# Kernel tuning notes

Hardware: AMD Instinct MI355X
Metric: run time of the kernel (lower is better)

The kernel has to match this reference:

```python
import jax, jax.numpy as jnp
import numpy as np

B, L, K = 16, 512, 30          # proteins, residues per protein, kNN neighbors
N = B * L
H, FC = 32, 3                  # h_channels, frame_channels
C = H + FC                     # fused sphere channels (35)
HEADS, AC, VC = 8, 16, 8       # heads, alpha channels (H//2), value channels (H//4)
RBF_N, POS_N = 16, 16
EF = RBF_N + POS_N

# idealized backbone atom positions (N, CA, C) in the local residue frame
IDEAL_BB = np.array([[-0.525, 1.363, 0.0], [0.0, 0.0, 0.0], [1.526, 0.0, 0.0]], dtype=np.float32)
# cartesian (x,y,z) -> real-SH l=1 ordering (y,z,x)
P_SH = np.array([[0., 1., 0.], [0., 0., 1.], [1., 0., 0.]], dtype=np.float32)


def _knn_edges(trans):
    # per-chain brute-force kNN (chains are contiguous blocks of length L)
    X = trans.reshape(B, L, 3)
    d2 = jnp.sum((X[:, :, None, :] - X[:, None, :, :]) ** 2, axis=-1)  # [B,L,L]
    d2 = d2 + jnp.eye(L, dtype=d2.dtype) * 1e9                          # exclude self
    _, idx = jax.lax.top_k(-d2, K)                                      # [B,L,K]
    off = (jnp.arange(B) * L)[:, None, None]
    src = (idx + off).reshape(-1)              # neighbor (edge_index[0])
    tgt = jnp.repeat(jnp.arange(N), K)         # center   (edge_index[1])
    return src, tgt


def _edge_rot_mat(vec):
    # rotation aligning the edge vector with the y axis (eSCN init_edge_rot_mat style)
    nx = vec / (jnp.linalg.norm(vec, axis=-1, keepdims=True) + 1e-12)
    ref = jnp.where(jnp.abs(nx[:, :1]) < 0.9,
                    jnp.array([1., 0., 0.], dtype=vec.dtype),
                    jnp.array([0., 0., 1.], dtype=vec.dtype))
    nz = jnp.cross(nx, ref)
    nz = nz / (jnp.linalg.norm(nz, axis=-1, keepdims=True) + 1e-12)
    ny = jnp.cross(nx, nz)
    ny = ny / (jnp.linalg.norm(ny, axis=-1, keepdims=True) + 1e-12)
    return jnp.stack([nz, nx, ny], axis=-2)  # [E,3,3]


def _rbf(d, d_min=0.0, d_max=20.0, count=RBF_N):
    mu = jnp.linspace(d_min, d_max, count)
    sigma = (d_max - d_min) / count
    return jnp.exp(-(((d[:, None] - mu) / sigma) ** 2))


def _pos_emb(src, tgt, num=POS_N):
    d = (src - tgt).astype(jnp.float32)
    freq = jnp.exp(jnp.arange(0, num, 2, dtype=jnp.float32) * (-np.log(10000.0) / num))
    ang = d[:, None] * freq
    return jnp.concatenate([jnp.cos(ang), jnp.sin(ang)], axis=-1)


def _forward(rots, trans, node_emb, batch, x_mask, noising_mask,
             W_alpha, a_vec, W_v, W_o, W_g, W_2):
    src, tgt = _knn_edges(trans)
    vec = trans[src] - trans[tgt]
    dist = jnp.linalg.norm(vec, axis=-1)
    valid = jnp.isfinite(dist) & (dist > 1e-3)  # edge_select, applied as mask

    R = _edge_rot_mat(vec)
    P = jnp.asarray(P_SH)
    D1 = jnp.einsum('ij,ejk,lk->eil', P, R, P)  # l=1 Wigner in real-SH basis [E,3,3]

    edge_features = jnp.concatenate([_rbf(dist), _pos_emb(src, tgt)], axis=-1)  # [E,32]

    # fuse node features with backbone frame atoms and editability flag
    frame_atoms = jnp.einsum('nij,aj->nai', rots, jnp.asarray(IDEAL_BB))  # [N,3atoms,3xyz]
    editable = noising_mask & (~x_mask)
    emb = jnp.zeros((N, 4, C), dtype=node_emb.dtype)
    emb = emb.at[:, :, :H].set(node_emb)
    emb = emb.at[:, 1:4, H:].set(jnp.swapaxes(frame_atoms, -1, -2))
    emb = emb.at[:, 0, C - 1].set(editable.astype(node_emb.dtype))

    # gather + rotate source features into edge frames
    xs = emb[src]                                                   # [E,4,C]
    xs_rot = jnp.concatenate([xs[:, :1], jnp.einsum('eij,ejc->eic', D1, xs[:, 1:])], axis=1)

    # invariant attention logits (l=0 of rotated src, l=0 of tgt, edge feats)
    inv = jnp.concatenate([xs_rot[:, 0], emb[tgt, 0], edge_features], axis=-1)  # [E,102]
    hdn = jax.nn.silu(inv @ W_alpha).reshape(-1, HEADS, AC)
    logits = jax.nn.leaky_relu(jnp.einsum('ehk,hk->eh', hdn, a_vec), 0.2)
    logits = jnp.where(valid[:, None], logits, -1e9)

    # segment softmax over incoming edges of each target node
    mx = jax.lax.stop_gradient(jax.ops.segment_max(logits, tgt, num_segments=N))
    ex = jnp.exp(logits - mx[tgt]) * valid[:, None].astype(logits.dtype)
    den = jax.ops.segment_sum(ex, tgt, num_segments=N)
    alpha = ex / (den[tgt] + 1e-9)                                  # [E,HEADS]

    # equivariant values, attention-weighted, rotate back, scatter
    v = (xs_rot @ W_v).reshape(-1, 4, HEADS, VC)
    m = (v * alpha[:, None, :, None]).reshape(-1, 4, HEADS * VC)
    m = jnp.concatenate([m[:, :1], jnp.einsum('eji,ejc->eic', D1, m[:, 1:])], axis=1)  # D^T
    agg = jax.ops.segment_sum(m, tgt, num_segments=N)               # [N,4,64]

    y = agg @ W_o                                                    # [N,4,H]
    gate = jax.nn.silu(y[:, 0] @ W_g)                                # invariant gating FFN
    return (y * gate[:, None, :]) @ W_2                              # [N,4,H]


def setup_inputs():
    key = jax.random.key(0)
    ks = jax.random.split(key, 12)
    rots = jax.vmap(lambda m: jnp.linalg.qr(m)[0])(jax.random.normal(ks[0], (N, 3, 3)))
    trans = jax.random.normal(ks[1], (N, 3)) * 10.0
    node_emb = jax.random.normal(ks[2], (N, 4, H))
    batch = jnp.repeat(jnp.arange(B, dtype=jnp.int32), L)
    x_mask = jax.random.randint(ks[3], (N,), 0, 2).astype(bool)
    noising_mask = jax.random.randint(ks[4], (N,), 0, 2).astype(bool)
    s = lambda k, sh, fan: jax.random.normal(k, sh) / np.sqrt(fan)
    return dict(rots=rots, trans=trans, node_emb=node_emb, batch=batch,
                x_mask=x_mask, noising_mask=noising_mask,
                W_alpha=s(ks[5], (2 * C + EF, HEADS * AC), 2 * C + EF),
                a_vec=s(ks[6], (HEADS, AC), AC),
                W_v=s(ks[7], (C, HEADS * VC), C),
                W_o=s(ks[8], (HEADS * VC, H), HEADS * VC),
                W_g=s(ks[9], (H, H), H),
                W_2=s(ks[10], (H, H), H))


def reference(rots, trans, node_emb, batch, x_mask, noising_mask,
              W_alpha, a_vec, W_v, W_o, W_g, W_2):
    return _forward(rots, trans, node_emb, batch, x_mask, noising_mask,
                    W_alpha, a_vec, W_v, W_o, W_g, W_2)
```

## Files before the change

kernel.cpp:

```cpp
#include <hip/hip_runtime.h>
#include <cstdint>

#define B_ 16
#define L_ 512
#define N_ 8192
#define K_ 30
#define E_ (N_*K_)
#define H_ 32
#define C_ 35

typedef uint16_t u16;
typedef uint32_t u32;
typedef unsigned long long u64;
typedef float f2v __attribute__((ext_vector_type(2)));

static __device__ __forceinline__ f2v splat2(float x) { f2v v; v.x = x; v.y = x; return v; }

static __device__ __forceinline__ float ldf(const void* p, int i, int bf) {
    return bf ? __uint_as_float(((u32)((const u16*)p)[i]) << 16)
              : ((const float*)p)[i];
}
static __device__ __forceinline__ float bfu16(u16 x) {
    return __uint_as_float(((u32)x) << 16);
}
static __device__ __forceinline__ int ldmask(const void* p, int i, int mode) {
    if (mode == 0) return ((const unsigned char*)p)[i] != 0;
    if (mode == 2) return ((const u32*)p)[2*i] != 0;
    return ((const u32*)p)[i] != 0;
}
static __device__ __forceinline__ u16 f2bf(float f) {
    u32 x = __float_as_uint(f);
    u32 r = x + 0x7FFFu + ((x >> 16) & 1u);
    return (u16)(r >> 16);
}
static __device__ __forceinline__ float fsilu(float x) {
    return x * __builtin_amdgcn_rcpf(1.f + __expf(-x));
}
static __device__ __forceinline__ float RL(float x, int i) {
    return __uint_as_float((u32)__builtin_amdgcn_readlane((int)__float_as_uint(x), i));
}

static __device__ __forceinline__ int detect_bf(const void* tr, int lane) {
    const u16* p = (const u16*)tr;
    int cnt = 0;
    for (int i = lane; i < 256; i += 64) {
        u16 v = p[2 * i];
        int e = (v >> 7) & 0xFF;
        if ((e >= 100 && e <= 141) || (v & 0x7FFFu) == 0) cnt++;
    }
    #pragma unroll
    for (int d = 1; d < 64; d <<= 1) cnt += __shfl_xor(cnt, d, 64);
    return cnt >= 192;
}
static __device__ __forceinline__ int detect_mm(const void* xmv, int lane) {
    const u32* xm = (const u32*)xmv;
    int anyBig = 0, oddNZ = 0;
    for (int i = lane; i < 1024; i += 64) {
        u32 w = xm[i];
        if (w & ~1u) anyBig = 1;
        if ((i & 1) && w) oddNZ = 1;
    }
    #pragma unroll
    for (int d = 1; d < 64; d <<= 1) {
        anyBig |= __shfl_xor(anyBig, d, 64);
        oddNZ  |= __shfl_xor(oddNZ, d, 64);
    }
    return anyBig ? 0 : (oddNZ ? 1 : 2);
}

__constant__ float cBB[9] = {-0.525f, 1.363f, 0.f,  0.f, 0.f, 0.f,  1.526f, 0.f, 0.f};

#define DPP_UMIN(var, CTRL) \
    { u32 o_ = (u32)__builtin_amdgcn_update_dpp((int)(var), (int)(var), CTRL, 0xF, 0xF, false); \
      (var) = (o_ < (var)) ? o_ : (var); }
#define DPP_UMIN_ALL(var) \
    DPP_UMIN(var, 0x111) DPP_UMIN(var, 0x112) DPP_UMIN(var, 0x114) \
    DPP_UMIN(var, 0x118) DPP_UMIN(var, 0x142) DPP_UMIN(var, 0x143)

#define DPP_ADD8(part) \
    part += __uint_as_float((u32)__builtin_amdgcn_update_dpp( \
        (int)__float_as_uint(part), (int)__float_as_uint(part), 0xB1, 0xF, 0xF, false)); \
    part += __uint_as_float((u32)__builtin_amdgcn_update_dpp( \
        (int)__float_as_uint(part), (int)__float_as_uint(part), 0x4E, 0xF, 0xF, false)); \
    part += __uint_as_float((u32)__builtin_amdgcn_update_dpp( \
        (int)__float_as_uint(part), (int)__float_as_uint(part), 0x141, 0xF, 0xF, false));

#define PKFMA_LO(acc, rr, w) \
    asm("v_pk_fma_f32 %0, %1, %2, %0 op_sel:[0,0,0] op_sel_hi:[0,1,1]" \
        : "+v"(acc) : "v"(rr), "v"(w))
#define PKFMA_HI(acc, rr, w) \
    asm("v_pk_fma_f32 %0, %1, %2, %0 op_sel:[1,0,0] op_sel_hi:[1,1,1]" \
        : "+v"(acc) : "v"(rr), "v"(w))

__global__ __launch_bounds__(256) void knn_prep_kernel(
    const void* __restrict__ rots, const void* __restrict__ trans,
    const void* __restrict__ node,
    const void* __restrict__ xm, const void* __restrict__ nm,
    const void* __restrict__ Wa, const void* __restrict__ av,
    const void* __restrict__ Wv, const void* __restrict__ Wo,
    const void* __restrict__ Wg, const void* __restrict__ W2,
    int* __restrict__ flag, int* __restrict__ srcArr,
    float* __restrict__ hsrc, float* __restrict__ htgt,
    float* __restrict__ ptab, float* __restrict__ V,
    float* __restrict__ c_wrb, float* __restrict__ c_av,
    float* __restrict__ c_Wo, float* __restrict__ c_Wg, float* __restrict__ c_W2)
{
    __shared__ float sX[L_], sY[L_], sZ[L_];
    __shared__ int flagS[2];
    const int bid = blockIdx.x, tid = threadIdx.x;
    const int lane = tid & 63, wid = tid >> 6;

    if (wid == 0) {
        int bfv = detect_bf(trans, lane);
        int mmv = 0;
        if (bid == 0 || (bid >= 2048 && bid < 4096)) mmv = detect_mm(xm, lane);
        if (bid == 0 && lane == 0) { flag[0] = bfv; flag[1] = mmv; }
        if (lane == 0) { flagS[0] = bfv; flagS[1] = mmv; }
    }
    __syncthreads();
    const int bf = flagS[0];

    if (bid < 2048) {
        const int t0 = bid * 4;
        const int base = (t0 >> 9) << 9;
        if (bf) {
            const u16* tp = (const u16*)trans;
            for (int i = tid; i < L_; i += 256) {
                sX[i] = bfu16(tp[(base + i) * 3 + 0]);
                sY[i] = bfu16(tp[(base + i) * 3 + 1]);
                sZ[i] = bfu16(tp[(base + i) * 3 + 2]);
            }
        } else {
            const float* tp = (const float*)trans;
            for (int i = tid; i < L_; i += 256) {
                sX[i] = tp[(base + i) * 3 + 0];
                sY[i] = tp[(base + i) * 3 + 1];
                sZ[i] = tp[(base + i) * 3 + 2];
            }
        }
        __syncthreads();

        const int t = t0 + wid;
        const int l = t & 511;
        const float tx = sX[l], ty = sY[l], tz = sZ[l];

        u32 d2b[8];
        #pragma unroll
        for (int i = 0; i < 8; ++i) {
            int j = lane + (i << 6);
            float dx = __fsub_rn(tx, sX[j]);
            float dy = __fsub_rn(ty, sY[j]);
            float dz = __fsub_rn(tz, sZ[j]);
            float d2 = __fadd_rn(__fadd_rn(__fmul_rn(dx, dx), __fmul_rn(dy, dy)), __fmul_rn(dz, dz));
            if (j == l) d2 = __fadd_rn(d2, 1e9f);
            d2b[i] = __float_as_uint(d2);
        }

        int myres = 0;
        for (int k = 0; k < K_; ++k) {
            u32 bb = d2b[0]; int bs = 0;
            #pragma unroll
            for (int i = 1; i < 8; ++i)
                if (d2b[i] < bb) { bb = d2b[i]; bs = i; }
            u32 m = bb;
            DPP_UMIN_ALL(m)
            u32 gbits = (u32)__builtin_amdgcn_readlane((int)m, 63);
            u64 mask = __ballot(bb == gbits);
            u32 gidx;
            if (__popcll(mask) == 1) {
                int wl = __ffsll((long long)mask) - 1;
                gidx = (u32)__builtin_amdgcn_readlane((int)((bs << 6) | lane), wl);
            } else {
                u32 cand = (bb == gbits) ? (u32)((bs << 6) | lane) : 0xFFFFFFFFu;
                DPP_UMIN_ALL(cand)
                gidx = (u32)__builtin_amdgcn_readlane((int)cand, 63);
            }
            if (lane == (u32)k) myres = (int)(gidx & 511u);
            if ((gidx & 63u) == (u32)lane) {
                int ws = (int)(gidx >> 6);
                #pragma unroll
                for (int i = 0; i < 8; ++i)
                    if (ws == i) d2b[i] = 0xFFFFFFFFu;
            }
        }
        if (lane < K_) srcArr[t * K_ + lane] = base + myres;

    } else if (bid < 4096) {
        const int mm = flagS[1];
        const int n = (bid - 2048) * 4 + wid;

        float eA, eB, eC = 0.f;
        {
            int s = lane;
            int r = s / 35, c = s - r * 35;
            if (c < H_)      eA = ldf(node, n * 128 + r * 32 + c, bf);
            else if (r == 0) eA = (c == 34) ? ((ldmask(nm, n, mm) && !ldmask(xm, n, mm)) ? 1.f : 0.f) : 0.f;
            else {
                int i = r - 1, a = c - 32;
                eA = ldf(rots, n*9 + i*3 + 0, bf) * cBB[a*3 + 0]
                   + ldf(rots, n*9 + i*3 + 1, bf) * cBB[a*3 + 1]
                   + ldf(rots, n*9 + i*3 + 2, bf) * cBB[a*3 + 2];
            }
            s = lane + 64;
            r = s / 35; c = s - r * 35;
            if (c < H_)      eB = ldf(node, n * 128 + r * 32 + c, bf);
            else {
                int i = r - 1, a = c - 32;
                eB = ldf(rots, n*9 + i*3 + 0, bf) * cBB[a*3 + 0]
                   + ldf(rots, n*9 + i*3 + 1, bf) * cBB[a*3 + 1]
                   + ldf(rots, n*9 + i*3 + 2, bf) * cBB[a*3 + 2];
            }
            if (lane < 12) {
                s = lane + 128;
                r = s / 35; c = s - r * 35;
                if (c < H_)      eC = ldf(node, n * 128 + r * 32 + c, bf);
                else {
                    int i = r - 1, a = c - 32;
                    eC = ldf(rots, n*9 + i*3 + 0, bf) * cBB[a*3 + 0]
                       + ldf(rots, n*9 + i*3 + 1, bf) * cBB[a*3 + 1]
                       + ldf(rots, n*9 + i*3 + 2, bf) * cBB[a*3 + 2];
                }
            }
        }

        float a0 = 0.f, a1 = 0.f, b0 = 0.f, b1 = 0.f;
        float v0 = 0.f, v1 = 0.f, v2 = 0.f, v3 = 0.f;
        if (bf) {
            const u16* wa = (const u16*)Wa;
            const u16* wv = (const u16*)Wv;
            #pragma unroll
            for (int i = 0; i < 35; ++i) {
                float ei = RL(eA, i);
                a0 = fmaf(ei, bfu16(wa[i * 128 + lane]),        a0);
                a1 = fmaf(ei, bfu16(wa[i * 128 + lane + 64]),   a1);
                b0 = fmaf(ei, bfu16(wa[(35 + i) * 128 + lane]),      b0);
                b1 = fmaf(ei, bfu16(wa[(35 + i) * 128 + lane + 64]), b1);
            }
            #pragma unroll
            for (int cp = 0; cp < 35; ++cp) {
                float w = bfu16(wv[cp * 64 + lane]);
                float e1 = (35 + cp < 64) ? RL(eA, 35 + cp) : RL(eB, cp - 29);
                float e3 = (cp < 23) ? RL(eB, 41 + cp) : RL(eC, cp - 23);
                v0 = fmaf(RL(eA, cp), w, v0);
                v1 = fmaf(e1, w, v1);
                v2 = fmaf(RL(eB, cp + 6), w, v2);
                v3 = fmaf(e3, w, v3);
            }
        } else {
            const float* wa = (const float*)Wa;
            const float* wv = (const float*)Wv;
            #pragma unroll
            for (int i = 0; i < 35; ++i) {
                float ei = RL(eA, i);
                a0 = fmaf(ei, wa[i * 128 + lane],        a0);
                a1 = fmaf(ei, wa[i * 128 + lane + 64],   a1);
                b0 = fmaf(ei, wa[(35 + i) * 128 + lane],      b0);
                b1 = fmaf(ei, wa[(35 + i) * 128 + lane + 64], b1);
            }
            #pragma unroll
            for (int cp = 0; cp < 35; ++cp) {
                float w = wv[cp * 64 + lane];
                float e1 = (35 + cp < 64) ? RL(eA, 35 + cp) : RL(eB, cp - 29);
                float e3 = (cp < 23) ? RL(eB, 41 + cp) : RL(eC, cp - 23);
                v0 = fmaf(RL(eA, cp), w, v0);
                v1 = fmaf(e1, w, v1);
                v2 = fmaf(RL(eB, cp + 6), w, v2);
                v3 = fmaf(e3, w, v3);
            }
        }
        hsrc[(size_t)n * 128 + lane]      = a0;
        hsrc[(size_t)n * 128 + lane + 64] = a1;
        htgt[(size_t)n * 128 + lane]      = b0;
        htgt[(size_t)n * 128 + lane + 64] = b1;
        float* vp = V + (size_t)n * 256 + lane;
        vp[0] = v0; vp[64] = v1; vp[128] = v2; vp[192] = v3;

    } else if (bid < 4608) {
        const int d   = (bid - 4096) * 2 + (tid >> 7);
        const int col = tid & 127;
        float dd = (float)(d - 512);
        float acc = 0.f;
        if (bf) {
            const u16* wa = (const u16*)Wa;
            #pragma unroll
            for (int q = 0; q < 8; ++q) {
                float fr = expf((float)(2 * q) * (-0.5756462732485115f));
                float ang = dd * fr;
                acc = fmaf(cosf(ang), bfu16(wa[(86 + q) * 128 + col]), acc);
                acc = fmaf(sinf(ang), bfu16(wa[(94 + q) * 128 + col]), acc);
            }
        } else {
            const float* wa = (const float*)Wa;
            #pragma unroll
            for (int q = 0; q < 8; ++q) {
                float fr = expf((float)(2 * q) * (-0.5756462732485115f));
                float ang = dd * fr;
                acc = fmaf(cosf(ang), wa[(86 + q) * 128 + col], acc);
                acc = fmaf(sinf(ang), wa[(94 + q) * 128 + col], acc);
            }
        }
        ptab[(size_t)d * 128 + col] = acc;

    } else {
        int g0 = (bid - 4608) * 256 + tid;
        for (int i = g0; i < 6272; i += 2048) {
            if      (i < 2048) c_wrb[i]        = ldf(Wa, 70 * 128 + i, bf);
            else if (i < 2176) c_av[i - 2048]  = ldf(av, i - 2048, bf);
            else if (i < 4224) c_Wo[i - 2176]  = ldf(Wo, i - 2176, bf);
            else if (i < 5248) c_Wg[i - 4224]  = ldf(Wg, i - 4224, bf);
            else               c_W2[i - 5248]  = ldf(W2, i - 5248, bf);
        }
    }
}

__global__ __launch_bounds__(256) void edge_agg_kernel(
    const void* __restrict__ trans, const int* __restrict__ srcArr,
    const float* __restrict__ hsrc, const float* __restrict__ htgt,
    const float* __restrict__ ptab, const float* __restrict__ V,
    const float* __restrict__ c_wrb, const float* __restrict__ c_av,
    const float* __restrict__ Wo, const float* __restrict__ Wg,
    const float* __restrict__ W2,
    const int* __restrict__ flag, void* __restrict__ outv)
{
    __shared__ __align__(16) float rbfS[K_][16];
    __shared__ float lgS[240];
    __shared__ int   hoffS[K_];
    __shared__ int   pdS[K_];
    __shared__ int   voffS[K_];
    __shared__ int   valS[K_];
    __shared__ float invS[8];
    __shared__ float aggS[256];
    __shared__ float ybuf[128];
    __shared__ float gbuf[32];

    const int bid = blockIdx.x, tid = threadIdx.x;
    const int lane = tid & 63, wid = tid >> 6;
    const int t = ((bid & 7) << 10) | (bid >> 3);
    const int bf = flag[0];

    const f2v* cw = (const f2v*)c_wrb;
    const f2v w0 = cw[0*64+lane],  w1 = cw[1*64+lane],  w2 = cw[2*64+lane],  w3 = cw[3*64+lane];
    const f2v w4 = cw[4*64+lane],  w5 = cw[5*64+lane],  w6 = cw[6*64+lane],  w7 = cw[7*64+lane];
    const f2v w8 = cw[8*64+lane],  w9 = cw[9*64+lane],  wA = cw[10*64+lane], wB = cw[11*64+lane];
    const f2v wC = cw[12*64+lane], wD = cw[13*64+lane], wE = cw[14*64+lane], wF = cw[15*64+lane];
    const f2v avv = ((const f2v*)c_av)[lane];
    const f2v ht  = *(const f2v*)(htgt + ((size_t)t << 7) + (lane << 1));

    if (tid < 240) {
        const int k  = tid >> 3;
        const int j2 = (tid & 7) << 1;
        int src = srcArr[t * K_ + k];
        src = (src < 0) ? 0 : ((src >= N_) ? (N_ - 1) : src);
        float vx = ldf(trans, src*3+0, bf) - ldf(trans, t*3+0, bf);
        float vy = ldf(trans, src*3+1, bf) - ldf(trans, t*3+1, bf);
        float vz = ldf(trans, src*3+2, bf) - ldf(trans, t*3+2, bf);
        float dist = sqrtf(vx*vx + vy*vy + vz*vz);
        bool valid = isfinite(dist) && (dist > 1e-3f);
        int d = src - t + 512;
        d = (d < 0) ? 0 : ((d > 1023) ? 1023 : d);
        float ta = (dist - (float)j2       * (20.f/15.f)) * 0.8f;
        float tb = (dist - (float)(j2 + 1) * (20.f/15.f)) * 0.8f;
        rbfS[k][j2]     = __expf(-ta * ta);
        rbfS[k][j2 + 1] = __expf(-tb * tb);
        if ((tid & 7) == 0) {
            hoffS[k] = src << 7;
            pdS[k]   = d << 7;
            voffS[k] = src << 8;
            valS[k]  = valid ? 1 : 0;
        }
    }
    __syncthreads();

    {
        const int kBeg = wid * 8;
        const int kEnd = (kBeg + 8 < K_) ? (kBeg + 8) : K_;
        #pragma unroll 2
        for (int k = kBeg; k < kEnd; ++k) {
            f2v hs = *(const f2v*)(hsrc + hoffS[k] + (lane << 1));
            f2v pt = *(const f2v*)(ptab + pdS[k]   + (lane << 1));
            f2v acc = (hs + ht) + pt;
            const float4* rp = (const float4*)(&rbfS[k][0]);
            float4 ra = rp[0], rb = rp[1], rc = rp[2], rd = rp[3];
            f2v r0; r0.x = ra.x; r0.y = ra.y;
            f2v r1; r1.x = ra.z; r1.y = ra.w;
            f2v r2; r2.x = rb.x; r2.y = rb.y;
            f2v r3; r3.x = rb.z; r3.y = rb.w;
            f2v r4; r4.x = rc.x; r4.y = rc.y;
            f2v r5; r5.x = rc.z; r5.y = rc.w;
            f2v r6; r6.x = rd.x; r6.y = rd.y;
            f2v r7; r7.x = rd.z; r7.y = rd.w;
            PKFMA_LO(acc, r0, w0); PKFMA_HI(acc, r0, w1);
            PKFMA_LO(acc, r1, w2); PKFMA_HI(acc, r1, w3);
            PKFMA_LO(acc, r2, w4); PKFMA_HI(acc, r2, w5);
            PKFMA_LO(acc, r3, w6); PKFMA_HI(acc, r3, w7);
            PKFMA_LO(acc, r4, w8); PKFMA_HI(acc, r4, w9);
            PKFMA_LO(acc, r5, wA); PKFMA_HI(acc, r5, wB);
            PKFMA_LO(acc, r6, wC); PKFMA_HI(acc, r6, wD);
            PKFMA_LO(acc, r7, wE); PKFMA_HI(acc, r7, wF);
            float part = fsilu(acc.x) * avv.x + fsilu(acc.y) * avv.y;
            DPP_ADD8(part)
            float lg = (part >= 0.f) ? part : 0.2f * part;
            if (!valS[k]) lg = -1e9f;
            lg = (fabsf(lg) < 1e30f) ? lg : -1e9f;
            if ((lane & 7) == 0) lgS[k * 8 + (lane >> 3)] = lg;
        }
    }
    __syncthreads();

    if (tid < 8) {
        float mx = -1e30f;
        #pragma unroll
        for (int k = 0; k < K_; ++k) mx = fmaxf(mx, lgS[k * 8 + tid]);
        float den = 0.f;
        #pragma unroll
        for (int k = 0; k < K_; ++k) {
            float l = lgS[k * 8 + tid];
            float e = (l > -1e8f) ? __expf(l - mx) : 0.f;
            lgS[k * 8 + tid] = e; den += e;
        }
        invS[tid] = 1.f / (den + 1e-9f);
    }
    __syncthreads();

    {
        const int h = (tid & 63) >> 3;
        float vv[K_];
        #pragma unroll
        for (int k = 0; k < K_; ++k) vv[k] = V[voffS[k] + tid];
        float acc = 0.f;
        #pragma unroll
        for (int k = 0; k < K_; ++k) acc = fmaf(lgS[k * 8 + h], vv[k], acc);
        aggS[tid] = acc * invS[h];
    }
    __syncthreads();

    if (tid < 128) {
        int rr = tid >> 5, o = tid & 31;
        float y = 0.f;
        #pragma unroll
        for (int c = 0; c < 64; ++c) y = fmaf(aggS[rr * 64 + c], Wo[c * 32 + o], y);
        ybuf[tid] = y;
    }
    __syncthreads();
    if (tid < 32) {
        float g = 0.f;
        #pragma unroll
        for (int o = 0; o < 32; ++o) g = fmaf(ybuf[o], Wg[o * 32 + tid], g);
        gbuf[tid] = fsilu(g);
    }
    __syncthreads();
    if (tid < 128) {
        int rr = tid >> 5, hh = tid & 31;
        float o = 0.f;
        #pragma unroll
        for (int g = 0; g < 32; ++g) o = fmaf(ybuf[rr * 32 + g] * gbuf[g], W2[g * 32 + hh], o);
        o = (fabsf(o) < 1e30f) ? o : 0.f;
        size_t idx = (size_t)t * 128 + tid;
        if (bf) ((u16*)outv)[idx] = f2bf(o);
        else    ((float*)outv)[idx] = o;
    }
}

extern "C" void kernel_launch(void* const* d_in, const int* in_sizes, int n_in,
                              void* d_out, int out_size, void* d_ws, size_t ws_size,
                              hipStream_t stream)
{
    const void* rots         = d_in[0];
    const void* trans        = d_in[1];
    const void* node_emb     = d_in[2];
    const void* x_mask       = d_in[4];
    const void* noising_mask = d_in[5];
    const void* Wa           = d_in[6];
    const void* avec         = d_in[7];
    const void* Wv           = d_in[8];
    const void* Wo           = d_in[9];
    const void* Wg           = d_in[10];
    const void* W2           = d_in[11];

    char* ws = (char*)d_ws;
    int*   flag    = (int*)  (ws + 0);
    int*   srcArr  = (int*)  (ws + 64);
    float* hsrc    = (float*)(ws + 983104);
    float* htgt    = (float*)(ws + 5177408);
    float* ptab    = (float*)(ws + 9371712);
    float* V       = (float*)(ws + 9896000);
    float* c_wrb   = (float*)(ws + 18284608);
    float* c_av    = (float*)(ws + 18292800);
    float* c_Wo    = (float*)(ws + 18293312);
    float* c_Wg    = (float*)(ws + 18301504);
    float* c_W2    = (float*)(ws + 18305600);

    hipLaunchKernelGGL(knn_prep_kernel, dim3(2048 + 2048 + 512 + 8), dim3(256), 0, stream,
                       rots, trans, node_emb, x_mask, noising_mask,
                       Wa, avec, Wv, Wo, Wg, W2,
                       flag, srcArr, hsrc, htgt, ptab, V,
                       c_wrb, c_av, c_Wo, c_Wg, c_W2);
    hipLaunchKernelGGL(edge_agg_kernel, dim3(N_), dim3(256), 0, stream,
                       trans, srcArr, hsrc, htgt, ptab, V,
                       c_wrb, c_av, c_Wo, c_Wg, c_W2, flag, d_out);
}
```

Measured before the change: 209.0 us.

## Map one wave per node in edge aggregation and merge prep block roles

The edge aggregation kernel now handles one target node per 64-lane wave, four nodes per block. Each wave has private shared buffers, and neighbour indices and validity are broadcast with readlane and ballot instead of going through shared memory. This removes the block-wide barriers between the logit, softmax, value-gather and output-MLP stages, and the V gather now uses paired float2 loads. The prep kernel is cut to 2048 blocks: each wave now does two kNN queries or two node projections, and the positional table and weight copies are folded into those same blocks. Both kernels also get an occupancy hint of 8 blocks per CU, which may force register spills.

Measured after the change: 515.8 us. 2.47x slower.

```diff
diff --git a/kernel.cpp b/kernel.cpp
--- a/kernel.cpp
+++ b/kernel.cpp
@@ -92,7 +92,7 @@
     asm("v_pk_fma_f32 %0, %1, %2, %0 op_sel:[1,0,0] op_sel_hi:[1,1,1]" \
         : "+v"(acc) : "v"(rr), "v"(w))
 
-__global__ __launch_bounds__(256) void knn_prep_kernel(
+__global__ __launch_bounds__(256, 8) void knn_prep_kernel(
     const void* __restrict__ rots, const void* __restrict__ trans,
     const void* __restrict__ node,
     const void* __restrict__ xm, const void* __restrict__ nm,
@@ -113,16 +113,16 @@
     if (wid == 0) {
         int bfv = detect_bf(trans, lane);
         int mmv = 0;
-        if (bid == 0 || (bid >= 2048 && bid < 4096)) mmv = detect_mm(xm, lane);
-        if (bid == 0 && lane == 0) { flag[0] = bfv; flag[1] = mmv; }
+        if (bid >= 1024) mmv = detect_mm(xm, lane);
+        if (bid == 0 && lane == 0) flag[0] = bfv;
         if (lane == 0) { flagS[0] = bfv; flagS[1] = mmv; }
     }
     __syncthreads();
     const int bf = flagS[0];
 
-    if (bid < 2048) {
-        const int t0 = bid * 4;
-        const int base = (t0 >> 9) << 9;
+    if (bid < 1024) {
+        const int t0 = bid * 8;
+        const int base = t0 & ~511;
         if (bf) {
             const u16* tp = (const u16*)trans;
             for (int i = tid; i < L_; i += 256) {
@@ -140,180 +140,187 @@
         }
         __syncthreads();
 
-        const int t = t0 + wid;
-        const int l = t & 511;
-        const float tx = sX[l], ty = sY[l], tz = sZ[l];
-
-        u32 d2b[8];
-        #pragma unroll
-        for (int i = 0; i < 8; ++i) {
-            int j = lane + (i << 6);
-            float dx = __fsub_rn(tx, sX[j]);
-            float dy = __fsub_rn(ty, sY[j]);
-            float dz = __fsub_rn(tz, sZ[j]);
-            float d2 = __fadd_rn(__fadd_rn(__fmul_rn(dx, dx), __fmul_rn(dy, dy)), __fmul_rn(dz, dz));
-            if (j == l) d2 = __fadd_rn(d2, 1e9f);
-            d2b[i] = __float_as_uint(d2);
-        }
-
-        int myres = 0;
-        for (int k = 0; k < K_; ++k) {
-            u32 bb = d2b[0]; int bs = 0;
+        for (int ti = 0; ti < 2; ++ti) {
+            const int t = t0 + wid + (ti << 2);
+            const int l = t & 511;
+            const float tx = sX[l], ty = sY[l], tz = sZ[l];
+
+            u32 d2b[8];
             #pragma unroll
-            for (int i = 1; i < 8; ++i)
-                if (d2b[i] < bb) { bb = d2b[i]; bs = i; }
-            u32 m = bb;
-            DPP_UMIN_ALL(m)
-            u32 gbits = (u32)__builtin_amdgcn_readlane((int)m, 63);
-            u64 mask = __ballot(bb == gbits);
-            u32 gidx;
-            if (__popcll(mask) == 1) {
-                int wl = __ffsll((long long)mask) - 1;
-                gidx = (u32)__builtin_amdgcn_readlane((int)((bs << 6) | lane), wl);
-            } else {
-                u32 cand = (bb == gbits) ? (u32)((bs << 6) | lane) : 0xFFFFFFFFu;
-                DPP_UMIN_ALL(cand)
-                gidx = (u32)__builtin_amdgcn_readlane((int)cand, 63);
-            }
-            if (lane == (u32)k) myres = (int)(gidx & 511u);
-            if ((gidx & 63u) == (u32)lane) {
-                int ws = (int)(gidx >> 6);
-                #pragma unroll
-                for (int i = 0; i < 8; ++i)
-                    if (ws == i) d2b[i] = 0xFFFFFFFFu;
-            }
-        }
-        if (lane < K_) srcArr[t * K_ + lane] = base + myres;
-
-    } else if (bid < 4096) {
+            for (int i = 0; i < 8; ++i) {
+                int j = lane + (i << 6);
+                float dx = __fsub_rn(tx, sX[j]);
+                float dy = __fsub_rn(ty, sY[j]);
+                float dz = __fsub_rn(tz, sZ[j]);
+                float d2 = __fadd_rn(__fadd_rn(__fmul_rn(dx, dx), __fmul_rn(dy, dy)), __fmul_rn(dz, dz));
+                if (j == l) d2 = __fadd_rn(d2, 1e9f);
+                d2b[i] = __float_as_uint(d2);
+            }
+
+            int myres = 0;
+            for (int k = 0; k < K_; ++k) {
+                u32 bb = d2b[0]; int bs = 0;
+                #pragma unroll
+                for (int i = 1; i < 8; ++i)
+                    if (d2b[i] < bb) { bb = d2b[i]; bs = i; }
+                u32 m = bb;
+                DPP_UMIN_ALL(m)
+                u32 gbits = (u32)__builtin_amdgcn_readlane((int)m, 63);
+                u64 mask = __ballot(bb == gbits);
+                u32 gidx;
+                if (__popcll(mask) == 1) {
+                    int wl = __ffsll((long long)mask) - 1;
+                    gidx = (u32)__builtin_amdgcn_readlane((int)((bs << 6) | lane), wl);
+                } else {
+                    u32 cand = (bb == gbits) ? (u32)((bs << 6) | lane) : 0xFFFFFFFFu;
+                    DPP_UMIN_ALL(cand)
+                    gidx = (u32)__builtin_amdgcn_readlane((int)cand, 63);
+                }
+                if (lane == (u32)k) myres = (int)(gidx & 511u);
+                if ((gidx & 63u) == (u32)lane) {
+                    int ws = (int)(gidx >> 6);
+                    #pragma unroll
+                    for (int i = 0; i < 8; ++i)
+                        if (ws == i) d2b[i] = 0xFFFFFFFFu;
+                }
+            }
+            if (lane < K_) srcArr[t * K_ + lane] = base + myres;
+        }
+
+        if (tid < 7) {
+            int i = bid * 7 + tid;
+            if (i < 6272) {
+                if      (i < 2048) c_wrb[i]        = ldf(Wa, 70 * 128 + i, bf);
+                else if (i < 2176) c_av[i - 2048]  = ldf(av, i - 2048, bf);
+                else if (i < 4224) c_Wo[i - 2176]  = ldf(Wo, i - 2176, bf);
+                else if (i < 5248) c_Wg[i - 4224]  = ldf(Wg, i - 4224, bf);
+                else               c_W2[i - 5248]  = ldf(W2, i - 5248, bf);
+            }
+        }
+
+    } else {
         const int mm = flagS[1];
-        const int n = (bid - 2048) * 4 + wid;
-
-        float eA, eB, eC = 0.f;
-        {
-            int s = lane;
-            int r = s / 35, c = s - r * 35;
-            if (c < H_)      eA = ldf(node, n * 128 + r * 32 + c, bf);
-            else if (r == 0) eA = (c == 34) ? ((ldmask(nm, n, mm) && !ldmask(xm, n, mm)) ? 1.f : 0.f) : 0.f;
-            else {
-                int i = r - 1, a = c - 32;
-                eA = ldf(rots, n*9 + i*3 + 0, bf) * cBB[a*3 + 0]
-                   + ldf(rots, n*9 + i*3 + 1, bf) * cBB[a*3 + 1]
-                   + ldf(rots, n*9 + i*3 + 2, bf) * cBB[a*3 + 2];
-            }
-            s = lane + 64;
-            r = s / 35; c = s - r * 35;
-            if (c < H_)      eB = ldf(node, n * 128 + r * 32 + c, bf);
-            else {
-                int i = r - 1, a = c - 32;
-                eB = ldf(rots, n*9 + i*3 + 0, bf) * cBB[a*3 + 0]
-                   + ldf(rots, n*9 + i*3 + 1, bf) * cBB[a*3 + 1]
-                   + ldf(rots, n*9 + i*3 + 2, bf) * cBB[a*3 + 2];
-            }
-            if (lane < 12) {
-                s = lane + 128;
-                r = s / 35; c = s - r * 35;
-                if (c < H_)      eC = ldf(node, n * 128 + r * 32 + c, bf);
+        const int nb = (bid - 1024) * 8;
+
+        for (int ni = 0; ni < 2; ++ni) {
+            const int n = nb + wid + (ni << 2);
+
+            float eA, eB, eC = 0.f;
+            {
+                int s = lane;
+                int r = s / 35, c = s - r * 35;
+                if (c < H_)      eA = ldf(node, n * 128 + r * 32 + c, bf);
+                else if (r == 0) eA = (c == 34) ? ((ldmask(nm, n, mm) && !ldmask(xm, n, mm)) ? 1.f : 0.f) : 0.f;
                 else {
                     int i = r - 1, a = c - 32;
-                    eC = ldf(rots, n*9 + i*3 + 0, bf) * cBB[a*3 + 0]
+                    eA = ldf(rots, n*9 + i*3 + 0, bf) * cBB[a*3 + 0]
                        + ldf(rots, n*9 + i*3 + 1, bf) * cBB[a*3 + 1]
                        + ldf(rots, n*9 + i*3 + 2, bf) * cBB[a*3 + 2];
                 }
-            }
-        }
-
-        float a0 = 0.f, a1 = 0.f, b0 = 0.f, b1 = 0.f;
-        float v0 = 0.f, v1 = 0.f, v2 = 0.f, v3 = 0.f;
-        if (bf) {
-            const u16* wa = (const u16*)Wa;
-            const u16* wv = (const u16*)Wv;
-            #pragma unroll
-            for (int i = 0; i < 35; ++i) {
-                float ei = RL(eA, i);
-                a0 = fmaf(ei, bfu16(wa[i * 128 + lane]),        a0);
-                a1 = fmaf(ei, bfu16(wa[i * 128 + lane + 64]),   a1);
-                b0 = fmaf(ei, bfu16(wa[(35 + i) * 128 + lane]),      b0);
-                b1 = fmaf(ei, bfu16(wa[(35 + i) * 128 + lane + 64]), b1);
-            }
-            #pragma unroll
-            for (int cp = 0; cp < 35; ++cp) {
-                float w = bfu16(wv[cp * 64 + lane]);
-                float e1 = (35 + cp < 64) ? RL(eA, 35 + cp) : RL(eB, cp - 29);
-                float e3 = (cp < 23) ? RL(eB, 41 + cp) : RL(eC, cp - 23);
-                v0 = fmaf(RL(eA, cp), w, v0);
-                v1 = fmaf(e1, w, v1);
-                v2 = fmaf(RL(eB, cp + 6), w, v2);
-                v3 = fmaf(e3, w, v3);
-            }
-        } else {
-            const float* wa = (const float*)Wa;
-            const float* wv = (const float*)Wv;
-            #pragma unroll
-            for (int i = 0; i < 35; ++i) {
-                float ei = RL(eA, i);
-                a0 = fmaf(ei, wa[i * 128 + lane],        a0);
-                a1 = fmaf(ei, wa[i * 128 + lane + 64],   a1);
-                b0 = fmaf(ei, wa[(35 + i) * 128 + lane],      b0);
-                b1 = fmaf(ei, wa[(35 + i) * 128 + lane + 64], b1);
-            }
-            #pragma unroll
-            for (int cp = 0; cp < 35; ++cp) {
-                float w = wv[cp * 64 + lane];
-                float e1 = (35 + cp < 64) ? RL(eA, 35 + cp) : RL(eB, cp - 29);
-                float e3 = (cp < 23) ? RL(eB, 41 + cp) : RL(eC, cp - 23);
-                v0 = fmaf(RL(eA, cp), w, v0);
-                v1 = fmaf(e1, w, v1);
-                v2 = fmaf(RL(eB, cp + 6), w, v2);
-                v3 = fmaf(e3, w, v3);
-            }
-        }
-        hsrc[(size_t)n * 128 + lane]      = a0;
-        hsrc[(size_t)n * 128 + lane + 64] = a1;
-        htgt[(size_t)n * 128 + lane]      = b0;
-        htgt[(size_t)n * 128 + lane + 64] = b1;
-        float* vp = V + (size_t)n * 256 + lane;
-        vp[0] = v0; vp[64] = v1; vp[128] = v2; vp[192] = v3;
-
-    } else if (bid < 4608) {
-        const int d   = (bid - 4096) * 2 + (tid >> 7);
-        const int col = tid & 127;
-        float dd = (float)(d - 512);
-        float acc = 0.f;
-        if (bf) {
-            const u16* wa = (const u16*)Wa;
-            #pragma unroll
-            for (int q = 0; q < 8; ++q) {
-                float fr = expf((float)(2 * q) * (-0.5756462732485115f));
-                float ang = dd * fr;
-                acc = fmaf(cosf(ang), bfu16(wa[(86 + q) * 128 + col]), acc);
-                acc = fmaf(sinf(ang), bfu16(wa[(94 + q) * 128 + col]), acc);
-            }
-        } else {
-            const float* wa = (const float*)Wa;
-            #pragma unroll
-            for (int q = 0; q < 8; ++q) {
-                float fr = expf((float)(2 * q) * (-0.5756462732485115f));
-                float ang = dd * fr;
-                acc = fmaf(cosf(ang), wa[(86 + q) * 128 + col], acc);
-                acc = fmaf(sinf(ang), wa[(94 + q) * 128 + col], acc);
-            }
-        }
-        ptab[(size_t)d * 128 + col] = acc;
-
-    } else {
-        int g0 = (bid - 4608) * 256 + tid;
-        for (int i = g0; i < 6272; i += 2048) {
-            if      (i < 2048) c_wrb[i]        = ldf(Wa, 70 * 128 + i, bf);
-            else if (i < 2176) c_av[i - 2048]  = ldf(av, i - 2048, bf);
-            else if (i < 4224) c_Wo[i - 2176]  = ldf(Wo, i - 2176, bf);
-            else if (i < 5248) c_Wg[i - 4224]  = ldf(Wg, i - 4224, bf);
-            else               c_W2[i - 5248]  = ldf(W2, i - 5248, bf);
-        }
-    }
-}
-
-__global__ __launch_bounds__(256) void edge_agg_kernel(
+                s = lane + 64;
+                r = s / 35; c = s - r * 35;
+                if (c < H_)      eB = ldf(node, n * 128 + r * 32 + c, bf);
+                else {
+                    int i = r - 1, a = c - 32;
+                    eB = ldf(rots, n*9 + i*3 + 0, bf) * cBB[a*3 + 0]
+                       + ldf(rots, n*9 + i*3 + 1, bf) * cBB[a*3 + 1]
+                       + ldf(rots, n*9 + i*3 + 2, bf) * cBB[a*3 + 2];
+                }
+                if (lane < 12) {
+                    s = lane + 128;
+                    r = s / 35; c = s - r * 35;
+                    if (c < H_)      eC = ldf(node, n * 128 + r * 32 + c, bf);
+                    else {
+                        int i = r - 1, a = c - 32;
+                        eC = ldf(rots, n*9 + i*3 + 0, bf) * cBB[a*3 + 0]
+                           + ldf(rots, n*9 + i*3 + 1, bf) * cBB[a*3 + 1]
+                           + ldf(rots, n*9 + i*3 + 2, bf) * cBB[a*3 + 2];
+                    }
+                }
+            }
+
+            float a0 = 0.f, a1 = 0.f, b0 = 0.f, b1 = 0.f;
+            float v0 = 0.f, v1 = 0.f, v2 = 0.f, v3 = 0.f;
+            if (bf) {
+                const u16* wa = (const u16*)Wa;
+                const u16* wv = (const u16*)Wv;
+                #pragma unroll
+                for (int i = 0; i < 35; ++i) {
+                    float ei = RL(eA, i);
+                    a0 = fmaf(ei, bfu16(wa[i * 128 + lane]),        a0);
+                    a1 = fmaf(ei, bfu16(wa[i * 128 + lane + 64]),   a1);
+                    b0 = fmaf(ei, bfu16(wa[(35 + i) * 128 + lane]),      b0);
+                    b1 = fmaf(ei, bfu16(wa[(35 + i) * 128 + lane + 64]), b1);
+                }
+                #pragma unroll
+                for (int cp = 0; cp < 35; ++cp) {
+                    float w = bfu16(wv[cp * 64 + lane]);
+                    float e1 = (35 + cp < 64) ? RL(eA, 35 + cp) : RL(eB, cp - 29);
+                    float e3 = (cp < 23) ? RL(eB, 41 + cp) : RL(eC, cp - 23);
+                    v0 = fmaf(RL(eA, cp), w, v0);
+                    v1 = fmaf(e1, w, v1);
+                    v2 = fmaf(RL(eB, cp + 6), w, v2);
+                    v3 = fmaf(e3, w, v3);
+                }
+            } else {
+                const float* wa = (const float*)Wa;
+                const float* wv = (const float*)Wv;
+                #pragma unroll
+                for (int i = 0; i < 35; ++i) {
+                    float ei = RL(eA, i);
+                    a0 = fmaf(ei, wa[i * 128 + lane],        a0);
+                    a1 = fmaf(ei, wa[i * 128 + lane + 64],   a1);
+                    b0 = fmaf(ei, wa[(35 + i) * 128 + lane],      b0);
+                    b1 = fmaf(ei, wa[(35 + i) * 128 + lane + 64], b1);
+                }
+                #pragma unroll
+                for (int cp = 0; cp < 35; ++cp) {
+                    float w = wv[cp * 64 + lane];
+                    float e1 = (35 + cp < 64) ? RL(eA, 35 + cp) : RL(eB, cp - 29);
+                    float e3 = (cp < 23) ? RL(eB, 41 + cp) : RL(eC, cp - 23);
+                    v0 = fmaf(RL(eA, cp), w, v0);
+                    v1 = fmaf(e1, w, v1);
+                    v2 = fmaf(RL(eB, cp + 6), w, v2);
+                    v3 = fmaf(e3, w, v3);
+                }
+            }
+            hsrc[(size_t)n * 128 + lane]      = a0;
+            hsrc[(size_t)n * 128 + lane + 64] = a1;
+            htgt[(size_t)n * 128 + lane]      = b0;
+            htgt[(size_t)n * 128 + lane + 64] = b1;
+            float* vp = V + (size_t)n * 256 + lane;
+            vp[0] = v0; vp[64] = v1; vp[128] = v2; vp[192] = v3;
+        }
+
+        const int d = bid - 1024;
+        if (tid < 128) {
+            float dd = (float)(d - 512);
+            float acc = 0.f;
+            if (bf) {
+                const u16* wa = (const u16*)Wa;
+                #pragma unroll
+                for (int q = 0; q < 8; ++q) {
+                    float fr = expf((float)(2 * q) * (-0.5756462732485115f));
+                    float ang = dd * fr;
+                    acc = fmaf(cosf(ang), bfu16(wa[(86 + q) * 128 + tid]), acc);
+                    acc = fmaf(sinf(ang), bfu16(wa[(94 + q) * 128 + tid]), acc);
+                }
+            } else {
+                const float* wa = (const float*)Wa;
+                #pragma unroll
+                for (int q = 0; q < 8; ++q) {
+                    float fr = expf((float)(2 * q) * (-0.5756462732485115f));
+                    float ang = dd * fr;
+                    acc = fmaf(cosf(ang), wa[(86 + q) * 128 + tid], acc);
+                    acc = fmaf(sinf(ang), wa[(94 + q) * 128 + tid], acc);
+                }
+            }
+            ptab[(size_t)d * 128 + tid] = acc;
+        }
+    }
+}
+
+__global__ __launch_bounds__(256, 8) void edge_agg_kernel(
     const void* __restrict__ trans, const int* __restrict__ srcArr,
     const float* __restrict__ hsrc, const float* __restrict__ htgt,
     const float* __restrict__ ptab, const float* __restrict__ V,
@@ -322,20 +329,17 @@
     const float* __restrict__ W2,
     const int* __restrict__ flag, void* __restrict__ outv)
 {
-    __shared__ __align__(16) float rbfS[K_][16];
-    __shared__ float lgS[240];
-    __shared__ int   hoffS[K_];
-    __shared__ int   pdS[K_];
-    __shared__ int   voffS[K_];
-    __shared__ int   valS[K_];
-    __shared__ float invS[8];
-    __shared__ float aggS[256];
-    __shared__ float ybuf[128];
-    __shared__ float gbuf[32];
+    __shared__ __align__(16) float rbfS[4][K_][16];
+    __shared__ float lgS[4][K_ * 8];
+    __shared__ float distS[4][32];
+    __shared__ float invS[4][8];
+    __shared__ float aggS[4][256];
+    __shared__ float ybS[4][128];
+    __shared__ float gbS[4][32];
 
     const int bid = blockIdx.x, tid = threadIdx.x;
     const int lane = tid & 63, wid = tid >> 6;
-    const int t = ((bid & 7) << 10) | (bid >> 3);
+    const int t = ((bid & 7) << 10) | ((bid >> 3) << 2) | wid;
     const int bf = flag[0];
 
     const f2v* cw = (const f2v*)c_wrb;
@@ -346,116 +350,128 @@
     const f2v avv = ((const f2v*)c_av)[lane];
     const f2v ht  = *(const f2v*)(htgt + ((size_t)t << 7) + (lane << 1));
 
-    if (tid < 240) {
-        const int k  = tid >> 3;
-        const int j2 = (tid & 7) << 1;
-        int src = srcArr[t * K_ + k];
-        src = (src < 0) ? 0 : ((src >= N_) ? (N_ - 1) : src);
+    int srcv = 0, dv = 0;
+    u64 vmask;
+    {
+        int src = 0;
+        if (lane < K_) {
+            src = srcArr[t * K_ + lane];
+            src = (src < 0) ? 0 : ((src >= N_) ? (N_ - 1) : src);
+        }
         float vx = ldf(trans, src*3+0, bf) - ldf(trans, t*3+0, bf);
         float vy = ldf(trans, src*3+1, bf) - ldf(trans, t*3+1, bf);
         float vz = ldf(trans, src*3+2, bf) - ldf(trans, t*3+2, bf);
         float dist = sqrtf(vx*vx + vy*vy + vz*vz);
         bool valid = isfinite(dist) && (dist > 1e-3f);
+        vmask = __ballot(valid);
+        srcv = src;
         int d = src - t + 512;
-        d = (d < 0) ? 0 : ((d > 1023) ? 1023 : d);
-        float ta = (dist - (float)j2       * (20.f/15.f)) * 0.8f;
-        float tb = (dist - (float)(j2 + 1) * (20.f/15.f)) * 0.8f;
-        rbfS[k][j2]     = __expf(-ta * ta);
-        rbfS[k][j2 + 1] = __expf(-tb * tb);
-        if ((tid & 7) == 0) {
-            hoffS[k] = src << 7;
-            pdS[k]   = d << 7;
-            voffS[k] = src << 8;
-            valS[k]  = valid ? 1 : 0;
-        }
-    }
-    __syncthreads();
-
-    {
-        const int kBeg = wid * 8;
-        const int kEnd = (kBeg + 8 < K_) ? (kBeg + 8) : K_;
-        #pragma unroll 2
-        for (int k = kBeg; k < kEnd; ++k) {
-            f2v hs = *(const f2v*)(hsrc + hoffS[k] + (lane << 1));
-            f2v pt = *(const f2v*)(ptab + pdS[k]   + (lane << 1));
-            f2v acc = (hs + ht) + pt;
-            const float4* rp = (const float4*)(&rbfS[k][0]);
-            float4 ra = rp[0], rb = rp[1], rc = rp[2], rd = rp[3];
-            f2v r0; r0.x = ra.x; r0.y = ra.y;
-            f2v r1; r1.x = ra.z; r1.y = ra.w;
-            f2v r2; r2.x = rb.x; r2.y = rb.y;
-            f2v r3; r3.x = rb.z; r3.y = rb.w;
-            f2v r4; r4.x = rc.x; r4.y = rc.y;
-            f2v r5; r5.x = rc.z; r5.y = rc.w;
-            f2v r6; r6.x = rd.x; r6.y = rd.y;
-            f2v r7; r7.x = rd.z; r7.y = rd.w;
-            PKFMA_LO(acc, r0, w0); PKFMA_HI(acc, r0, w1);
-            PKFMA_LO(acc, r1, w2); PKFMA_HI(acc, r1, w3);
-            PKFMA_LO(acc, r2, w4); PKFMA_HI(acc, r2, w5);
-            PKFMA_LO(acc, r3, w6); PKFMA_HI(acc, r3, w7);
-            PKFMA_LO(acc, r4, w8); PKFMA_HI(acc, r4, w9);
-            PKFMA_LO(acc, r5, wA); PKFMA_HI(acc, r5, wB);
-            PKFMA_LO(acc, r6, wC); PKFMA_HI(acc, r6, wD);
-            PKFMA_LO(acc, r7, wE); PKFMA_HI(acc, r7, wF);
-            float part = fsilu(acc.x) * avv.x + fsilu(acc.y) * avv.y;
-            DPP_ADD8(part)
-            float lg = (part >= 0.f) ? part : 0.2f * part;
-            if (!valS[k]) lg = -1e9f;
-            lg = (fabsf(lg) < 1e30f) ? lg : -1e9f;
-            if ((lane & 7) == 0) lgS[k * 8 + (lane >> 3)] = lg;
-        }
-    }
-    __syncthreads();
-
-    if (tid < 8) {
+        dv = (d < 0) ? 0 : ((d > 1023) ? 1023 : d);
+        if (lane < 32) distS[wid][lane] = dist;
+    }
+
+    #pragma unroll
+    for (int it = 0; it < 8; ++it) {
+        int e = lane + (it << 6);
+        if (e < 480) {
+            int k = e >> 4, j = e & 15;
+            float dd = distS[wid][k];
+            float tt = (dd - (float)j * (20.f/15.f)) * 0.8f;
+            rbfS[wid][k][j] = __expf(-tt * tt);
+        }
+    }
+
+    #pragma unroll 2
+    for (int k = 0; k < K_; ++k) {
+        const int src = __builtin_amdgcn_readlane(srcv, k);
+        const int d   = __builtin_amdgcn_readlane(dv, k);
+        f2v hs = *(const f2v*)(hsrc + ((size_t)src << 7) + (lane << 1));
+        f2v pt = *(const f2v*)(ptab + ((size_t)d << 7) + (lane << 1));
+        f2v acc = (hs + ht) + pt;
+        const float4* rp = (const float4*)(&rbfS[wid][k][0]);
+        float4 ra = rp[0], rb = rp[1], rc = rp[2], rd = rp[3];
+        f2v r0; r0.x = ra.x; r0.y = ra.y;
+        f2v r1; r1.x = ra.z; r1.y = ra.w;
+        f2v r2; r2.x = rb.x; r2.y = rb.y;
+        f2v r3; r3.x = rb.z; r3.y = rb.w;
+        f2v r4; r4.x = rc.x; r4.y = rc.y;
+        f2v r5; r5.x = rc.z; r5.y = rc.w;
+        f2v r6; r6.x = rd.x; r6.y = rd.y;
+        f2v r7; r7.x = rd.z; r7.y = rd.w;
+        PKFMA_LO(acc, r0, w0); PKFMA_HI(acc, r0, w1);
+        PKFMA_LO(acc, r1, w2); PKFMA_HI(acc, r1, w3);
+        PKFMA_LO(acc, r2, w4); PKFMA_HI(acc, r2, w5);
+        PKFMA_LO(acc, r3, w6); PKFMA_HI(acc, r3, w7);
+        PKFMA_LO(acc, r4, w8); PKFMA_HI(acc, r4, w9);
+        PKFMA_LO(acc, r5, wA); PKFMA_HI(acc, r5, wB);
+        PKFMA_LO(acc, r6, wC); PKFMA_HI(acc, r6, wD);
+        PKFMA_LO(acc, r7, wE); PKFMA_HI(acc, r7, wF);
+        float part = fsilu(acc.x) * avv.x + fsilu(acc.y) * avv.y;
+        DPP_ADD8(part)
+        float lg = (part >= 0.f) ? part : 0.2f * part;
+        if (!((vmask >> k) & 1ull)) lg = -1e9f;
+        lg = (fabsf(lg) < 1e30f) ? lg : -1e9f;
+        if ((lane & 7) == 0) lgS[wid][k * 8 + (lane >> 3)] = lg;
+    }
+
+    if (lane < 8) {
         float mx = -1e30f;
         #pragma unroll
-        for (int k = 0; k < K_; ++k) mx = fmaxf(mx, lgS[k * 8 + tid]);
+        for (int k = 0; k < K_; ++k) mx = fmaxf(mx, lgS[wid][k * 8 + lane]);
         float den = 0.f;
         #pragma unroll
         for (int k = 0; k < K_; ++k) {
-            float l = lgS[k * 8 + tid];
+            float l = lgS[wid][k * 8 + lane];
             float e = (l > -1e8f) ? __expf(l - mx) : 0.f;
-            lgS[k * 8 + tid] = e; den += e;
-        }
-        invS[tid] = 1.f / (den + 1e-9f);
-    }
-    __syncthreads();
+            lgS[wid][k * 8 + lane] = e; den += e;
+        }
+        invS[wid][lane] = 1.f / (den + 1e-9f);
+    }
 
     {
-        const int h = (tid & 63) >> 3;
-        float vv[K_];
+        const int h = (lane & 31) >> 2;
+        f2v a0; a0.x = 0.f; a0.y = 0.f;
+        f2v a1; a1.x = 0.f; a1.y = 0.f;
         #pragma unroll
-        for (int k = 0; k < K_; ++k) vv[k] = V[voffS[k] + tid];
-        float acc = 0.f;
-        #pragma unroll
-        for (int k = 0; k < K_; ++k) acc = fmaf(lgS[k * 8 + h], vv[k], acc);
-        aggS[tid] = acc * invS[h];
-    }
-    __syncthreads();
-
-    if (tid < 128) {
-        int rr = tid >> 5, o = tid & 31;
+        for (int k = 0; k < K_; ++k) {
+            const int src = __builtin_amdgcn_readlane(srcv, k);
+            const float* vr = V + ((size_t)src << 8) + (lane << 1);
+            f2v w = splat2(lgS[wid][k * 8 + h]);
+            f2v x0 = *(const f2v*)(vr);
+            f2v x1 = *(const f2v*)(vr + 128);
+            a0 = __builtin_elementwise_fma(w, x0, a0);
+            a1 = __builtin_elementwise_fma(w, x1, a1);
+        }
+        const float inv = invS[wid][h];
+        a0.x *= inv; a0.y *= inv; a1.x *= inv; a1.y *= inv;
+        *(f2v*)&aggS[wid][(lane << 1)]       = a0;
+        *(f2v*)&aggS[wid][(lane << 1) + 128] = a1;
+    }
+
+    #pragma unroll
+    for (int p = 0; p < 2; ++p) {
+        const int rr = (p << 1) | (lane >> 5);
+        const int o  = lane & 31;
         float y = 0.f;
         #pragma unroll
-        for (int c = 0; c < 64; ++c) y = fmaf(aggS[rr * 64 + c], Wo[c * 32 + o], y);
-        ybuf[tid] = y;
-    }
-    __syncthreads();
-    if (tid < 32) {
+        for (int c = 0; c < 64; ++c) y = fmaf(aggS[wid][rr * 64 + c], Wo[c * 32 + o], y);
+        ybS[wid][rr * 32 + o] = y;
+    }
+    if (lane < 32) {
         float g = 0.f;
         #pragma unroll
-        for (int o = 0; o < 32; ++o) g = fmaf(ybuf[o], Wg[o * 32 + tid], g);
-        gbuf[tid] = fsilu(g);
-    }
-    __syncthreads();
-    if (tid < 128) {
-        int rr = tid >> 5, hh = tid & 31;
+        for (int o = 0; o < 32; ++o) g = fmaf(ybS[wid][o], Wg[o * 32 + lane], g);
+        gbS[wid][lane] = fsilu(g);
+    }
+    #pragma unroll
+    for (int p = 0; p < 2; ++p) {
+        const int rr = (p << 1) | (lane >> 5);
+        const int hh = lane & 31;
         float o = 0.f;
         #pragma unroll
-        for (int g = 0; g < 32; ++g) o = fmaf(ybuf[rr * 32 + g] * gbuf[g], W2[g * 32 + hh], o);
+        for (int g = 0; g < 32; ++g) o = fmaf(ybS[wid][rr * 32 + g] * gbS[wid][g], W2[g * 32 + hh], o);
         o = (fabsf(o) < 1e30f) ? o : 0.f;
-        size_t idx = (size_t)t * 128 + tid;
+        size_t idx = (size_t)t * 128 + (p << 6) + lane;
         if (bf) ((u16*)outv)[idx] = f2bf(o);
         else    ((float*)outv)[idx] = o;
     }
@@ -490,12 +506,12 @@
     float* c_Wg    = (float*)(ws + 18301504);
     float* c_W2    = (float*)(ws + 18305600);
 
-    hipLaunchKernelGGL(knn_prep_kernel, dim3(2048 + 2048 + 512 + 8), dim3(256), 0, stream,
+    hipLaunchKernelGGL(knn_prep_kernel, dim3(2048), dim3(256), 0, stream,
                        rots, trans, node_emb, x_mask, noising_mask,
                        Wa, avec, Wv, Wo, Wg, W2,
                        flag, srcArr, hsrc, htgt, ptab, V,
                        c_wrb, c_av, c_Wo, c_Wg, c_W2);
-    hipLaunchKernelGGL(edge_agg_kernel, dim3(N_), dim3(256), 0, stream,
+    hipLaunchKernelGGL(edge_agg_kernel, dim3(2048), dim3(256), 0, stream,
                        trans, srcArr, hsrc, htgt, ptab, V,
                        c_wrb, c_av, c_Wo, c_Wg, c_W2, flag, d_out);
 }
```
